# Kernel optimization log

Measured on AMD Instinct MI355X. Metric: run time of the kernel, lower is better.

Reference implementation:

```python
import jax, jax.numpy as jnp
import numpy as np

N = 8192       # paired user/item batch
D_IN = 10000   # interaction-vector length
H = 1024       # hidden width
E = 128        # shared embedding dim


def setup_inputs() -> dict:
    key = jax.random.key(0)
    ks = jax.random.split(key, 10)
    g = 5.0 / 3.0  # tanh gain used by the torch init

    def xavier(k, shape):
        fan_in, fan_out = shape
        std = g * np.sqrt(2.0 / (fan_in + fan_out))
        return jax.random.normal(k, shape, dtype=jnp.float32) * std

    return {
        "user_data": jax.random.normal(ks[0], (N, D_IN), dtype=jnp.float32),
        "item_data": jax.random.normal(ks[1], (N, D_IN), dtype=jnp.float32),
        "Wu1": xavier(ks[2], (D_IN, H)),
        "bu1": jnp.full((H,), 0.01, dtype=jnp.float32),
        "Wu2": xavier(ks[3], (H, E)),
        "bu2": jnp.full((E,), 0.01, dtype=jnp.float32),
        "Wi1": xavier(ks[4], (D_IN, H)),
        "bi1": jnp.full((H,), 0.01, dtype=jnp.float32),
        "Wi2": xavier(ks[5], (H, E)),
        "bi2": jnp.full((E,), 0.01, dtype=jnp.float32),
    }


def reference(user_data, item_data, Wu1, bu1, Wu2, bu2, Wi1, bi1, Wi2, bi2):
    # Encoders (dropout is identity at inference). PolyLinear: Linear -> ReLU -> Linear.
    p = jax.nn.relu(user_data @ Wu1 + bu1) @ Wu2 + bu2   # [N, E]
    q = jax.nn.relu(item_data @ Wi1 + bi1) @ Wi2 + bi2   # [N, E]
    # (p @ q.T).diag() == row-wise dot product; identical math, O(N*E) not O(N^2*E).
    return jnp.einsum("ne,ne->n", p, q)
```

## Files before the change

### kernel.cpp

```cpp
#include <hip/hip_runtime.h>
#include <hip/hip_bf16.h>
#include <stdint.h>

#define KP   10112
#define DIN  10000
#define NB   8192
#define HID  1024
#define EMB  128
#define NI   79

typedef __attribute__((ext_vector_type(8))) __bf16 bf16x8;
typedef __attribute__((ext_vector_type(4))) float  f32x4;
typedef __attribute__((ext_vector_type(4))) unsigned short ushort4v;

typedef const __attribute__((address_space(1))) void* gas_cp;
typedef __attribute__((address_space(3))) void* las_p;

__device__ __forceinline__ unsigned short f2bf(float f) {
    union { float f; unsigned u; } c; c.f = f;
    unsigned u = c.u;
    u += 0x7FFFu + ((u >> 16) & 1u);
    return (unsigned short)(u >> 16);
}

__global__ void conv_pad2(const float* __restrict__ user, const float* __restrict__ item,
                          unsigned short* __restrict__ dst) {
    const int c4  = blockIdx.x * blockDim.x + threadIdx.x;
    const int row = blockIdx.y;
    const int side = blockIdx.z;
    if (c4 >= KP / 4) return;
    const float* src = side ? item : user;
    unsigned short* d = dst + (size_t)side * NB * KP;
    ushort4v o;
    if (c4 < DIN / 4) {
        float4 a = *(const float4*)(src + (size_t)row * DIN + (size_t)c4 * 4);
        o[0] = f2bf(a.x); o[1] = f2bf(a.y); o[2] = f2bf(a.z); o[3] = f2bf(a.w);
    } else {
        o[0] = o[1] = o[2] = o[3] = 0;
    }
    *(ushort4v*)(d + (size_t)row * KP + (size_t)c4 * 4) = o;
}

__global__ void conv_transpose(const float* __restrict__ src, unsigned short* __restrict__ dst,
                               int K, int N, int Kp) {
    __shared__ float tile[64][33];
    const int tx = threadIdx.x & 31, ty = threadIdx.x >> 5;
    const int k0 = blockIdx.x * 64, n0 = blockIdx.y * 32;
#pragma unroll
    for (int j = 0; j < 8; ++j) {
        int k = k0 + ty + j * 8;
        tile[ty + j * 8][tx] = (k < K) ? src[(size_t)k * N + n0 + tx] : 0.0f;
    }
    __syncthreads();
#pragma unroll
    for (int j = 0; j < 4; ++j) {
        int n = n0 + ty + j * 8;
        unsigned short lo = f2bf(tile[2 * tx][ty + j * 8]);
        unsigned short hi = f2bf(tile[2 * tx + 1][ty + j * 8]);
        unsigned int packed = (unsigned int)lo | ((unsigned int)hi << 16);
        *(unsigned int*)(dst + (size_t)n * Kp + k0 + 2 * tx) = packed;
    }
}

#define DSR(d, ad, off) asm volatile("ds_read_b128 %0, %1 offset:" off : "=v"(d) : "v"(ad))
#define GATE(n) do { asm volatile("s_waitcnt lgkmcnt(" #n ")" ::: "memory"); \
                     __builtin_amdgcn_sched_barrier(0); } while (0)

__global__ __launch_bounds__(512, 2)
void gemm1_4p(const unsigned short* __restrict__ Abf,
              const unsigned short* __restrict__ W1t,
              const float* __restrict__ b1u, const float* __restrict__ b1i,
              unsigned short* __restrict__ H1) {
    __shared__ __align__(16) unsigned short lds_[81920];

    const int t  = threadIdx.x;
    const int lane = t & 63, wv = t >> 6;
    const int wm = wv >> 2, wn = wv & 3;
    const int rA = lane & 15, kg = lane >> 4;

    const int id   = blockIdx.y * 8 + blockIdx.x;
    const int pos  = (id & 7) * 32 + (id >> 3);
    const int bm   = pos >> 3;
    const int bxc  = pos & 7;
    const int side = bxc >> 2, bn = bxc & 3;

    const unsigned short* AbfS = Abf + (size_t)side * NB * KP;
    const unsigned short* W1tS = W1t + (size_t)side * HID * KP;
    const float* bias = side ? b1i : b1u;
    unsigned short* Cout = H1 + (size_t)side * NB * HID;

    const int rowSA = bm * 256 + (t >> 3);
    const int rowSB = bn * 256 + (t >> 3);
    const int kcl   = ((t & 7) ^ ((t >> 3) & 7)) * 8;

    const int xk0 = ((0 * 4 + kg) ^ (rA & 7)) * 8;
    const int xk1 = ((1 * 4 + kg) ^ (rA & 7)) * 8;

    const unsigned ldsB = (unsigned)(size_t)lds_;
    const unsigned aC0 = ldsB + wm * 16384 + rA * 128 + xk0 * 2;
    const unsigned aC1 = ldsB + wm * 16384 + rA * 128 + xk1 * 2;
    const unsigned bC0 = ldsB + 98304 + (wn >> 1) * 16384 + (wn & 1) * 8192 + rA * 128 + xk0 * 2;
    const unsigned bC1 = ldsB + 98304 + (wn >> 1) * 16384 + (wn & 1) * 8192 + rA * 128 + xk1 * 2;

    f32x4 acc[8][4] = {};
    bf16x8 a[4][2], b[4][2];

    auto stA = [&](int tile, int h, int buf) {
        const unsigned short* s = AbfS + (size_t)(rowSA + h * 128) * KP + tile * 64 + kcl;
        __builtin_amdgcn_global_load_lds((gas_cp)s, (las_p)(lds_ + buf * 16384 + h * 8192 + wv * 512), 16, 0, 0);
        __builtin_amdgcn_global_load_lds((gas_cp)(s + (size_t)64 * KP), (las_p)(lds_ + buf * 16384 + h * 8192 + 4096 + wv * 512), 16, 0, 0);
    };
    auto stB = [&](int tile, int h, int par) {
        const unsigned short* s = W1tS + (size_t)(rowSB + h * 128) * KP + tile * 64 + kcl;
        __builtin_amdgcn_global_load_lds((gas_cp)s, (las_p)(lds_ + 49152 + par * 16384 + h * 8192 + wv * 512), 16, 0, 0);
        __builtin_amdgcn_global_load_lds((gas_cp)(s + (size_t)64 * KP), (las_p)(lds_ + 49152 + par * 16384 + h * 8192 + 4096 + wv * 512), 16, 0, 0);
    };

    auto rdB01 = [&](int par) {
        unsigned b0 = bC0 + par * 32768, b1 = bC1 + par * 32768;
        DSR(b[0][0], b0, "0");    DSR(b[0][1], b1, "0");
        DSR(b[1][0], b0, "2048"); DSR(b[1][1], b1, "2048");
    };
    auto rdB23 = [&](int par) {
        unsigned b0 = bC0 + par * 32768 + 4096, b1 = bC1 + par * 32768 + 4096;
        DSR(b[2][0], b0, "0");    DSR(b[2][1], b1, "0");
        DSR(b[3][0], b0, "2048"); DSR(b[3][1], b1, "2048");
    };
    auto rdA4 = [&](int buf, int mq) {
        unsigned a0 = aC0 + buf * 32768 + mq * 8192, a1 = aC1 + buf * 32768 + mq * 8192;
        DSR(a[0][0], a0, "0");    DSR(a[0][1], a1, "0");
        DSR(a[1][0], a0, "2048"); DSR(a[1][1], a1, "2048");
        DSR(a[2][0], a0, "4096"); DSR(a[2][1], a1, "4096");
        DSR(a[3][0], a0, "6144"); DSR(a[3][1], a1, "6144");
    };
    auto mmj = [&](int mq, int j, int nq) {
        acc[mq*4+j][nq*2+0] = __builtin_amdgcn_mfma_f32_16x16x32_bf16(a[j][0], b[nq*2+0][0], acc[mq*4+j][nq*2+0], 0, 0, 0);
        acc[mq*4+j][nq*2+0] = __builtin_amdgcn_mfma_f32_16x16x32_bf16(a[j][1], b[nq*2+0][1], acc[mq*4+j][nq*2+0], 0, 0, 0);
        acc[mq*4+j][nq*2+1] = __builtin_amdgcn_mfma_f32_16x16x32_bf16(a[j][0], b[nq*2+1][0], acc[mq*4+j][nq*2+1], 0, 0, 0);
        acc[mq*4+j][nq*2+1] = __builtin_amdgcn_mfma_f32_16x16x32_bf16(a[j][1], b[nq*2+1][1], acc[mq*4+j][nq*2+1], 0, 0, 0);
    };
    auto mmcol = [&](int mq, int col) {
#pragma unroll
        for (int j = 0; j < 4; ++j) {
            acc[mq*4+j][col] = __builtin_amdgcn_mfma_f32_16x16x32_bf16(a[j][0], b[col][0], acc[mq*4+j][col], 0, 0, 0);
            acc[mq*4+j][col] = __builtin_amdgcn_mfma_f32_16x16x32_bf16(a[j][1], b[col][1], acc[mq*4+j][col], 0, 0, 0);
        }
    };

    stA(0, 0, 0); stA(0, 1, 0);
    stB(0, 0, 0); stB(0, 1, 0);
    stA(1, 0, 1); stA(1, 1, 1);
    asm volatile("s_waitcnt vmcnt(4)" ::: "memory");
    __builtin_amdgcn_s_barrier();

    int cA0 = 0, cA1 = 1, nA = 2;
    for (int i = 0; i < NI - 1; ++i) {
        const int T1 = 2 * i + 1, S0 = 2 * i + 2, S1 = 2 * i + 3;
        rdB01(0); rdA4(cA0, 0); rdB23(0);
        stB(T1, 0, 1); stB(T1, 1, 1);
        __builtin_amdgcn_s_setprio(1);
        GATE(10); mmj(0,0,0); GATE(8); mmj(0,1,0); GATE(6); mmj(0,2,0);
        GATE(4);  mmj(0,3,0); GATE(2); mmcol(0,2); GATE(0); mmcol(0,3);
        __builtin_amdgcn_s_setprio(0);
        __builtin_amdgcn_s_barrier();
        rdA4(cA0, 1);
        stA(S0, 0, nA); stA(S0, 1, nA);
        __builtin_amdgcn_s_setprio(1);
        GATE(6); mmj(1,0,0); GATE(4); mmj(1,1,0); GATE(2); mmj(1,2,0);
        GATE(0); mmj(1,3,0); mmcol(1,2); mmcol(1,3);
        __builtin_amdgcn_s_setprio(0);
        asm volatile("s_waitcnt vmcnt(4)" ::: "memory");
        __builtin_amdgcn_s_barrier();
        rdB01(1); rdA4(cA1, 0); rdB23(1);
        stB(S0, 0, 0); stB(S0, 1, 0);
        __builtin_amdgcn_s_setprio(1);
        GATE(10); mmj(0,0,0); GATE(8); mmj(0,1,0); GATE(6); mmj(0,2,0);
        GATE(4);  mmj(0,3,0); GATE(2); mmcol(0,2); GATE(0); mmcol(0,3);
        __builtin_amdgcn_s_setprio(0);
        __builtin_amdgcn_s_barrier();
        rdA4(cA1, 1);
        stA(S1, 0, cA0); stA(S1, 1, cA0);
        __builtin_amdgcn_s_setprio(1);
        GATE(6); mmj(1,0,0); GATE(4); mmj(1,1,0); GATE(2); mmj(1,2,0);
        GATE(0); mmj(1,3,0); mmcol(1,2); mmcol(1,3);
        __builtin_amdgcn_s_setprio(0);
        asm volatile("s_waitcnt vmcnt(4)" ::: "memory");
        __builtin_amdgcn_s_barrier();
        int tmp = cA1; cA1 = cA0; cA0 = nA; nA = tmp;
    }
    {
        const int TL = 2 * NI - 1;
        rdB01(0); rdA4(cA0, 0); rdB23(0);
        stB(TL, 0, 1); stB(TL, 1, 1);
        __builtin_amdgcn_s_setprio(1);
        GATE(10); mmj(0,0,0); GATE(8); mmj(0,1,0); GATE(6); mmj(0,2,0);
        GATE(4);  mmj(0,3,0); GATE(2); mmcol(0,2); GATE(0); mmcol(0,3);
        __builtin_amdgcn_s_setprio(0);
        __builtin_amdgcn_s_barrier();
        rdA4(cA0, 1);
        __builtin_amdgcn_s_setprio(1);
        GATE(6); mmj(1,0,0); GATE(4); mmj(1,1,0); GATE(2); mmj(1,2,0);
        GATE(0); mmj(1,3,0); mmcol(1,2); mmcol(1,3);
        __builtin_amdgcn_s_setprio(0);
        asm volatile("s_waitcnt vmcnt(0)" ::: "memory");
        __builtin_amdgcn_s_barrier();
        rdB01(1); rdA4(cA1, 0); rdB23(1);
        __builtin_amdgcn_s_setprio(1);
        GATE(10); mmj(0,0,0); GATE(8); mmj(0,1,0); GATE(6); mmj(0,2,0);
        GATE(4);  mmj(0,3,0); GATE(2); mmcol(0,2); GATE(0); mmcol(0,3);
        __builtin_amdgcn_s_setprio(0);
        __builtin_amdgcn_s_barrier();
        rdA4(cA1, 1);
        __builtin_amdgcn_s_setprio(1);
        GATE(6); mmj(1,0,0); GATE(4); mmj(1,1,0); GATE(2); mmj(1,2,0);
        GATE(0); mmj(1,3,0); mmcol(1,2); mmcol(1,3);
        __builtin_amdgcn_s_setprio(0);
    }

    const int rowbase = bm * 256 + wm * 128 + kg * 4;
    const int colbase = bn * 256 + wn * 64 + rA;
#pragma unroll
    for (int ni = 0; ni < 4; ++ni) {
        const int col = colbase + ni * 16;
        const float bv = bias[col];
#pragma unroll
        for (int mi = 0; mi < 8; ++mi) {
#pragma unroll
            for (int rr = 0; rr < 4; ++rr) {
                float v = fmaxf(acc[mi][ni][rr] + bv, 0.0f);
                Cout[(size_t)(rowbase + mi * 16 + rr) * HID + col] = f2bf(v);
            }
        }
    }
}

__global__ __launch_bounds__(256, 2)
void gemm2k(const unsigned short* __restrict__ H1,
            const unsigned short* __restrict__ W2t,
            const float* __restrict__ b2u, const float* __restrict__ b2i,
            float* __restrict__ PQh) {
    __shared__ unsigned short As[3 * 4096];
    __shared__ unsigned short Bs[3 * 4096];

    const int t = threadIdx.x, lane = t & 63, wave = t >> 6;
    const int wr = wave >> 1, wc = wave & 1, rA = lane & 15, kg = lane >> 4;
    const int kh = blockIdx.x, bm = blockIdx.y, side = blockIdx.z;
    const int nk = 512 / 32;

    const unsigned short* A  = H1  + (size_t)side * NB * HID + kh * 512;
    const unsigned short* Bt = W2t + (size_t)side * EMB * HID + kh * 512;
    const float* bias = side ? b2i : b2u;
    float* Cout = PQh + (size_t)(kh * 2 + side) * NB * EMB;

    const int srcc = (t & 3) ^ ((t >> 3) & 3);
    const unsigned short* ga = A  + (size_t)(bm * 128 + (t >> 2)) * HID + (size_t)srcc * 8;
    const unsigned short* gb = Bt + (size_t)(t >> 2) * HID + (size_t)srcc * 8;
    const size_t aP = (size_t)64 * HID;

    f32x4 acc[4][4] = {};
    const int swz  = (rA >> 1) & 3;
    const int aoff = (wr * 64 + rA) * 32 + (kg ^ swz) * 8;
    const int boff = (wc * 64 + rA) * 32 + (kg ^ swz) * 8;
    const int wst  = wave * 512;

    auto stage = [&](int buf) {
        const int bo = buf << 12;
        __builtin_amdgcn_global_load_lds((gas_cp)(ga),      (las_p)(As + bo + wst),        16, 0, 0);
        __builtin_amdgcn_global_load_lds((gas_cp)(ga + aP), (las_p)(As + bo + wst + 2048), 16, 0, 0);
        __builtin_amdgcn_global_load_lds((gas_cp)(gb),      (las_p)(Bs + bo + wst),        16, 0, 0);
        __builtin_amdgcn_global_load_lds((gas_cp)(gb + aP), (las_p)(Bs + bo + wst + 2048), 16, 0, 0);
        ga += 32; gb += 32;
    };
    auto compute = [&](int buf) {
        const int bo = buf << 12;
        bf16x8 af[4], bfr[4];
#pragma unroll
        for (int m = 0; m < 4; ++m) af[m]  = *(const bf16x8*)(As + bo + aoff + m * 512);
#pragma unroll
        for (int n = 0; n < 4; ++n) bfr[n] = *(const bf16x8*)(Bs + bo + boff + n * 512);
#pragma unroll
        for (int m = 0; m < 4; ++m)
#pragma unroll
            for (int n = 0; n < 4; ++n)
                acc[m][n] = __builtin_amdgcn_mfma_f32_16x16x32_bf16(af[m], bfr[n], acc[m][n], 0, 0, 0);
    };

    stage(0); stage(1);
    int cur = 0;
    for (int kt = 0; kt < nk - 2; ++kt) {
        int pfb = cur + 2; if (pfb >= 3) pfb -= 3;
        stage(pfb);
        asm volatile("s_waitcnt vmcnt(8)" ::: "memory");
        __builtin_amdgcn_s_barrier();
        compute(cur);
        __builtin_amdgcn_s_barrier();
        cur = (cur + 1 == 3) ? 0 : cur + 1;
    }
    asm volatile("s_waitcnt vmcnt(4)" ::: "memory");
    __builtin_amdgcn_s_barrier();
    compute(cur);
    cur = (cur + 1 == 3) ? 0 : cur + 1;
    asm volatile("s_waitcnt vmcnt(0)" ::: "memory");
    __builtin_amdgcn_s_barrier();
    compute(cur);

    const int rowbase = bm * 128 + wr * 64 + kg * 4;
    const int colbase = wc * 64 + rA;
#pragma unroll
    for (int n = 0; n < 4; ++n) {
        const int col = colbase + n * 16;
        const float bv = (kh == 0) ? bias[col] : 0.0f;
#pragma unroll
        for (int m = 0; m < 4; ++m) {
#pragma unroll
            for (int r = 0; r < 4; ++r) {
                Cout[(size_t)(rowbase + m * 16 + r) * EMB + col] = acc[m][n][r] + bv;
            }
        }
    }
}

__global__ void rowdot4(const float* __restrict__ PQh, float* __restrict__ out, int n) {
    int gid = blockIdx.x * blockDim.x + threadIdx.x;
    int w = gid >> 6, lane = gid & 63;
    if (w >= n) return;
    const size_t C = (size_t)NB * EMB;
    const float2 p0 = ((const float2*)(PQh + 0 * C + (size_t)w * EMB))[lane];
    const float2 q0 = ((const float2*)(PQh + 1 * C + (size_t)w * EMB))[lane];
    const float2 p1 = ((const float2*)(PQh + 2 * C + (size_t)w * EMB))[lane];
    const float2 q1 = ((const float2*)(PQh + 3 * C + (size_t)w * EMB))[lane];
    const float px = p0.x + p1.x, py = p0.y + p1.y;
    const float qx = q0.x + q1.x, qy = q0.y + q1.y;
    float s = px * qx + py * qy;
#pragma unroll
    for (int off = 32; off; off >>= 1) s += __shfl_down(s, off);
    if (lane == 0) out[w] = s;
}

extern "C" void kernel_launch(void* const* d_in, const int* in_sizes, int n_in,
                              void* d_out, int out_size, void* d_ws, size_t ws_size,
                              hipStream_t stream) {
    const float* user = (const float*)d_in[0];
    const float* item = (const float*)d_in[1];
    const float* Wu1  = (const float*)d_in[2];
    const float* bu1  = (const float*)d_in[3];
    const float* Wu2  = (const float*)d_in[4];
    const float* bu2  = (const float*)d_in[5];
    const float* Wi1  = (const float*)d_in[6];
    const float* bi1  = (const float*)d_in[7];
    const float* Wi2  = (const float*)d_in[8];
    const float* bi2  = (const float*)d_in[9];
    float* out = (float*)d_out;

    char* ws = (char*)d_ws;
    size_t off = 0;
    auto alloc = [&](size_t bytes) {
        char* p = ws + off;
        off += (bytes + 255) & ~(size_t)255;
        return p;
    };

    unsigned short* W1t = (unsigned short*)alloc((size_t)2 * HID * KP * 2);
    unsigned short* W2t = (unsigned short*)alloc((size_t)2 * EMB * HID * 2);
    float* PQh = (float*)alloc((size_t)4 * NB * EMB * 4);
    unsigned short* H1 = (unsigned short*)alloc((size_t)2 * NB * HID * 2);
    unsigned short* Abf = (unsigned short*)alloc((size_t)2 * NB * KP * 2);

    dim3 blk(256);
    conv_transpose<<<dim3(KP / 64, HID / 32), blk, 0, stream>>>(Wu1, W1t,                      DIN, HID, KP);
    conv_transpose<<<dim3(KP / 64, HID / 32), blk, 0, stream>>>(Wi1, W1t + (size_t)HID * KP,   DIN, HID, KP);
    conv_transpose<<<dim3(HID / 64, EMB / 32), blk, 0, stream>>>(Wu2, W2t,                     HID, EMB, HID);
    conv_transpose<<<dim3(HID / 64, EMB / 32), blk, 0, stream>>>(Wi2, W2t + (size_t)EMB * HID, HID, EMB, HID);

    conv_pad2<<<dim3((KP / 4 + 255) / 256, NB, 2), blk, 0, stream>>>(user, item, Abf);
    gemm1_4p<<<dim3(8, 32), dim3(512), 0, stream>>>(Abf, W1t, bu1, bi1, H1);
    gemm2k<<<dim3(2, 64, 2), blk, 0, stream>>>(H1, W2t, bu2, bi2, PQh);
    rowdot4<<<(NB * 64) / 256, blk, 0, stream>>>(PQh, out, NB);
}
```

Measured before the change: 482.5 us.

## Merge GEMM1 half-phases into one phase with double-buffered A fragment registers

Each K-step's two halves (mq=0 and mq=1) become a single phase with no workgroup barrier between them. The LDS reads for the second A fragment set go into a separate register array (a2) and are issued while the first half's MFMAs are still running, so the LDS latency can overlap compute. This halves the barriers per K-tile and lets the next-tile global-to-LDS A loads issue earlier. In exchange, 32 more VGPRs are live under a 512-thread, 2-blocks-per-CU bound, which could cause spills or lower occupancy.

After: 483.1 us. No clear change (+0.1%).

```diff
diff --git a/kernel.cpp b/kernel.cpp
--- a/kernel.cpp
+++ b/kernel.cpp
@@ -67,7 +67,7 @@
                      __builtin_amdgcn_sched_barrier(0); } while (0)
 
 __global__ __launch_bounds__(512, 2)
-void gemm1_4p(const unsigned short* __restrict__ Abf,
+void gemm1_2p(const unsigned short* __restrict__ Abf,
               const unsigned short* __restrict__ W1t,
               const float* __restrict__ b1u, const float* __restrict__ b1i,
               unsigned short* __restrict__ H1) {
@@ -103,7 +103,7 @@
     const unsigned bC1 = ldsB + 98304 + (wn >> 1) * 16384 + (wn & 1) * 8192 + rA * 128 + xk1 * 2;
 
     f32x4 acc[8][4] = {};
-    bf16x8 a[4][2], b[4][2];
+    bf16x8 a[4][2], a2[4][2], b[4][2];
 
     auto stA = [&](int tile, int h, int buf) {
         const unsigned short* s = AbfS + (size_t)(rowSA + h * 128) * KP + tile * 64 + kcl;
@@ -127,11 +127,18 @@
         DSR(b[3][0], b0, "2048"); DSR(b[3][1], b1, "2048");
     };
     auto rdA4 = [&](int buf, int mq) {
-        unsigned a0 = aC0 + buf * 32768 + mq * 8192, a1 = aC1 + buf * 32768 + mq * 8192;
-        DSR(a[0][0], a0, "0");    DSR(a[0][1], a1, "0");
-        DSR(a[1][0], a0, "2048"); DSR(a[1][1], a1, "2048");
-        DSR(a[2][0], a0, "4096"); DSR(a[2][1], a1, "4096");
-        DSR(a[3][0], a0, "6144"); DSR(a[3][1], a1, "6144");
+        unsigned p0 = aC0 + buf * 32768 + mq * 8192, p1 = aC1 + buf * 32768 + mq * 8192;
+        DSR(a[0][0], p0, "0");    DSR(a[0][1], p1, "0");
+        DSR(a[1][0], p0, "2048"); DSR(a[1][1], p1, "2048");
+        DSR(a[2][0], p0, "4096"); DSR(a[2][1], p1, "4096");
+        DSR(a[3][0], p0, "6144"); DSR(a[3][1], p1, "6144");
+    };
+    auto rdA4_2 = [&](int buf, int mq) {
+        unsigned p0 = aC0 + buf * 32768 + mq * 8192, p1 = aC1 + buf * 32768 + mq * 8192;
+        DSR(a2[0][0], p0, "0");    DSR(a2[0][1], p1, "0");
+        DSR(a2[1][0], p0, "2048"); DSR(a2[1][1], p1, "2048");
+        DSR(a2[2][0], p0, "4096"); DSR(a2[2][1], p1, "4096");
+        DSR(a2[3][0], p0, "6144"); DSR(a2[3][1], p1, "6144");
     };
     auto mmj = [&](int mq, int j, int nq) {
         acc[mq*4+j][nq*2+0] = __builtin_amdgcn_mfma_f32_16x16x32_bf16(a[j][0], b[nq*2+0][0], acc[mq*4+j][nq*2+0], 0, 0, 0);
@@ -146,6 +153,34 @@
             acc[mq*4+j][col] = __builtin_amdgcn_mfma_f32_16x16x32_bf16(a[j][1], b[col][1], acc[mq*4+j][col], 0, 0, 0);
         }
     };
+    auto mmj2 = [&](int mq, int j, int nq) {
+        acc[mq*4+j][nq*2+0] = __builtin_amdgcn_mfma_f32_16x16x32_bf16(a2[j][0], b[nq*2+0][0], acc[mq*4+j][nq*2+0], 0, 0, 0);
+        acc[mq*4+j][nq*2+0] = __builtin_amdgcn_mfma_f32_16x16x32_bf16(a2[j][1], b[nq*2+0][1], acc[mq*4+j][nq*2+0], 0, 0, 0);
+        acc[mq*4+j][nq*2+1] = __builtin_amdgcn_mfma_f32_16x16x32_bf16(a2[j][0], b[nq*2+1][0], acc[mq*4+j][nq*2+1], 0, 0, 0);
+        acc[mq*4+j][nq*2+1] = __builtin_amdgcn_mfma_f32_16x16x32_bf16(a2[j][1], b[nq*2+1][1], acc[mq*4+j][nq*2+1], 0, 0, 0);
+    };
+    auto mmcol2 = [&](int mq, int col) {
+#pragma unroll
+        for (int j = 0; j < 4; ++j) {
+            acc[mq*4+j][col] = __builtin_amdgcn_mfma_f32_16x16x32_bf16(a2[j][0], b[col][0], acc[mq*4+j][col], 0, 0, 0);
+            acc[mq*4+j][col] = __builtin_amdgcn_mfma_f32_16x16x32_bf16(a2[j][1], b[col][1], acc[mq*4+j][col], 0, 0, 0);
+        }
+    };
+
+    auto phase = [&](int bufA, int parB, bool doB, int tB, int pB,
+                     bool doA, int tA, int bA) {
+        rdB01(parB); rdA4(bufA, 0); rdB23(parB);
+        if (doB) { stB(tB, 0, pB); stB(tB, 1, pB); }
+        __builtin_amdgcn_s_setprio(1);
+        GATE(10); mmj(0,0,0); GATE(8); mmj(0,1,0); GATE(6); mmj(0,2,0);
+        GATE(4);  mmj(0,3,0); GATE(2); mmcol(0,2);
+        rdA4_2(bufA, 1);
+        if (doA) { stA(tA, 0, bA); stA(tA, 1, bA); }
+        GATE(8);  mmcol(0,3);
+        GATE(6);  mmj2(1,0,0); GATE(4); mmj2(1,1,0); GATE(2); mmj2(1,2,0);
+        GATE(0);  mmj2(1,3,0); mmcol2(1,2); mmcol2(1,3);
+        __builtin_amdgcn_s_setprio(0);
+    };
 
     stA(0, 0, 0); stA(0, 1, 0);
     stB(0, 0, 0); stB(0, 1, 0);
@@ -156,65 +191,20 @@
     int cA0 = 0, cA1 = 1, nA = 2;
     for (int i = 0; i < NI - 1; ++i) {
         const int T1 = 2 * i + 1, S0 = 2 * i + 2, S1 = 2 * i + 3;
-        rdB01(0); rdA4(cA0, 0); rdB23(0);
-        stB(T1, 0, 1); stB(T1, 1, 1);
-        __builtin_amdgcn_s_setprio(1);
-        GATE(10); mmj(0,0,0); GATE(8); mmj(0,1,0); GATE(6); mmj(0,2,0);
-        GATE(4);  mmj(0,3,0); GATE(2); mmcol(0,2); GATE(0); mmcol(0,3);
-        __builtin_amdgcn_s_setprio(0);
-        __builtin_amdgcn_s_barrier();
-        rdA4(cA0, 1);
-        stA(S0, 0, nA); stA(S0, 1, nA);
-        __builtin_amdgcn_s_setprio(1);
-        GATE(6); mmj(1,0,0); GATE(4); mmj(1,1,0); GATE(2); mmj(1,2,0);
-        GATE(0); mmj(1,3,0); mmcol(1,2); mmcol(1,3);
-        __builtin_amdgcn_s_setprio(0);
+        phase(cA0, 0, true, T1, 1, true, S0, nA);
         asm volatile("s_waitcnt vmcnt(4)" ::: "memory");
         __builtin_amdgcn_s_barrier();
-        rdB01(1); rdA4(cA1, 0); rdB23(1);
-        stB(S0, 0, 0); stB(S0, 1, 0);
-        __builtin_amdgcn_s_setprio(1);
-        GATE(10); mmj(0,0,0); GATE(8); mmj(0,1,0); GATE(6); mmj(0,2,0);
-        GATE(4);  mmj(0,3,0); GATE(2); mmcol(0,2); GATE(0); mmcol(0,3);
-        __builtin_amdgcn_s_setprio(0);
-        __builtin_amdgcn_s_barrier();
-        rdA4(cA1, 1);
-        stA(S1, 0, cA0); stA(S1, 1, cA0);
-        __builtin_amdgcn_s_setprio(1);
-        GATE(6); mmj(1,0,0); GATE(4); mmj(1,1,0); GATE(2); mmj(1,2,0);
-        GATE(0); mmj(1,3,0); mmcol(1,2); mmcol(1,3);
-        __builtin_amdgcn_s_setprio(0);
+        phase(cA1, 1, true, S0, 0, true, S1, cA0);
         asm volatile("s_waitcnt vmcnt(4)" ::: "memory");
         __builtin_amdgcn_s_barrier();
         int tmp = cA1; cA1 = cA0; cA0 = nA; nA = tmp;
     }
     {
         const int TL = 2 * NI - 1;
-        rdB01(0); rdA4(cA0, 0); rdB23(0);
-        stB(TL, 0, 1); stB(TL, 1, 1);
-        __builtin_amdgcn_s_setprio(1);
-        GATE(10); mmj(0,0,0); GATE(8); mmj(0,1,0); GATE(6); mmj(0,2,0);
-        GATE(4);  mmj(0,3,0); GATE(2); mmcol(0,2); GATE(0); mmcol(0,3);
-        __builtin_amdgcn_s_setprio(0);
-        __builtin_amdgcn_s_barrier();
-        rdA4(cA0, 1);
-        __builtin_amdgcn_s_setprio(1);
-        GATE(6); mmj(1,0,0); GATE(4); mmj(1,1,0); GATE(2); mmj(1,2,0);
-        GATE(0); mmj(1,3,0); mmcol(1,2); mmcol(1,3);
-        __builtin_amdgcn_s_setprio(0);
+        phase(cA0, 0, true, TL, 1, false, 0, 0);
         asm volatile("s_waitcnt vmcnt(0)" ::: "memory");
         __builtin_amdgcn_s_barrier();
-        rdB01(1); rdA4(cA1, 0); rdB23(1);
-        __builtin_amdgcn_s_setprio(1);
-        GATE(10); mmj(0,0,0); GATE(8); mmj(0,1,0); GATE(6); mmj(0,2,0);
-        GATE(4);  mmj(0,3,0); GATE(2); mmcol(0,2); GATE(0); mmcol(0,3);
-        __builtin_amdgcn_s_setprio(0);
-        __builtin_amdgcn_s_barrier();
-        rdA4(cA1, 1);
-        __builtin_amdgcn_s_setprio(1);
-        GATE(6); mmj(1,0,0); GATE(4); mmj(1,1,0); GATE(2); mmj(1,2,0);
-        GATE(0); mmj(1,3,0); mmcol(1,2); mmcol(1,3);
-        __builtin_amdgcn_s_setprio(0);
+        phase(cA1, 1, false, 0, 0, false, 0, 0);
     }
 
     const int rowbase = bm * 256 + wm * 128 + kg * 4;
@@ -373,7 +363,7 @@
     conv_transpose<<<dim3(HID / 64, EMB / 32), blk, 0, stream>>>(Wi2, W2t + (size_t)EMB * HID, HID, EMB, HID);
 
     conv_pad2<<<dim3((KP / 4 + 255) / 256, NB, 2), blk, 0, stream>>>(user, item, Abf);
-    gemm1_4p<<<dim3(8, 32), dim3(512), 0, stream>>>(Abf, W1t, bu1, bi1, H1);
+    gemm1_2p<<<dim3(8, 32), dim3(512), 0, stream>>>(Abf, W1t, bu1, bi1, H1);
     gemm2k<<<dim3(2, 64, 2), blk, 0, stream>>>(H1, W2t, bu2, bi2, PQh);
     rowdot4<<<(NB * 64) / 256, blk, 0, stream>>>(PQh, out, NB);
 }
```
